# Optimization experiments

Measured on AMD Instinct MI355X. Metric: run time of the kernel, lower is better.

The kernel has to match this reference:

```python
import jax, jax.numpy as jnp
import numpy as np

NZ = 128
N_GEN = 8
BATCH = 2048
SLOPE = 0.2


def _convt(x, w, b, stride, pad):
    # PyTorch ConvTranspose2d(weight [Cin,Cout,kH,kW], stride, padding p)
    # == conv with lhs_dilation=stride, padding=k-1-p, spatially-flipped
    # kernel with in/out channels swapped.
    k = jnp.flip(w, axis=(2, 3)).transpose(2, 3, 0, 1)  # [kH,kW,Cin,Cout]
    y = jax.lax.conv_general_dilated(
        x, k, window_strides=(1, 1), padding=[(pad, pad), (pad, pad)],
        lhs_dilation=(stride, stride),
        dimension_numbers=('NCHW', 'HWIO', 'NCHW'))
    return y + b[None, :, None, None]


def setup_inputs() -> dict:
    key = jax.random.key(0)
    ks = jax.random.split(key, 12)
    s = 0.05
    return {
        'z': jax.random.normal(ks[0], (BATCH, NZ), jnp.float32),
        'g_idx': jax.random.randint(ks[1], (BATCH,), 0, N_GEN),
        'W1': jax.random.normal(ks[2], (N_GEN, NZ, 256), jnp.float32) * s,
        'b1': jax.random.normal(ks[3], (N_GEN, 256), jnp.float32) * s,
        'W2': jax.random.normal(ks[4], (N_GEN, 256, 1568), jnp.float32) * s,
        'b2': jax.random.normal(ks[5], (N_GEN, 1568), jnp.float32) * s,
        'cw1': jax.random.normal(ks[6], (N_GEN, 32, 16, 4, 4), jnp.float32) * s,
        'cb1': jax.random.normal(ks[7], (N_GEN, 16), jnp.float32) * s,
        'cw2': jax.random.normal(ks[8], (N_GEN, 16, 8, 4, 4), jnp.float32) * s,
        'cb2': jax.random.normal(ks[9], (N_GEN, 8), jnp.float32) * s,
        'cw3': jax.random.normal(ks[10], (N_GEN, 8, 1, 3, 3), jnp.float32) * s,
        'cb3': jax.random.normal(ks[11], (N_GEN, 1), jnp.float32) * s,
    }


def _single_gen(params, z):
    W1, b1, W2, b2, cw1, cb1, cw2, cb2, cw3, cb3 = params
    lrelu = lambda x: jax.nn.leaky_relu(x, SLOPE)
    h = lrelu(z @ W1 + b1)                 # [B,256]
    h = lrelu(h @ W2 + b2)                 # [B,1568]
    h = h.reshape(-1, 32, 7, 7)
    h = lrelu(_convt(h, cw1, cb1, 2, 2))   # [B,16,14,14]
    h = lrelu(_convt(h, cw2, cb2, 2, 2))   # [B,8,28,28]
    return jnp.tanh(_convt(h, cw3, cb3, 1, 1))  # [B,1,28,28]


def reference(z, g_idx, W1, b1, W2, b2, cw1, cb1, cw2, cb2, cw3, cb3):
    params = (W1, b1, W2, b2, cw1, cb1, cw2, cb2, cw3, cb3)
    # Compute every generator on the full batch (faithful to the torch loop),
    # vmapped over the generator axis: images [G,B,1,28,28].
    images = jax.vmap(_single_gen, in_axes=((0,) * 10, None))(params, z)
    # Per-sample gather: keep generator g_idx[b] for each sample b.
    return images[g_idx, jnp.arange(z.shape[0])]
```

## Files before the change

### kernel.cpp

```cpp
#include <hip/hip_runtime.h>
#include <cstdint>
#include <cstddef>

#define BATCH 2048
#define NZ 128
#define NGEN 8
#define GRPS 32
#define MAXG 72
#define NCT 7
#define H2_ELEMS 1792
#define WS_H1_OFF 16384
#define WS_H2_OFF (16384 + MAXG * 8192 * 4)
#define WS_W2T_OFF (WS_H2_OFF + BATCH * H2_ELEMS * 2)
#define W2T_GSTRIDE (1568 * 256)
#define NB_W2T (NGEN * 49)
#define NB_PREP (NB_W2T + MAXG * 4)
#define WS_WPK1_OFF (WS_W2T_OFF + NGEN * W2T_GSTRIDE * 2)
#define WS_WPK2_OFF (WS_WPK1_OFF + NGEN * 8192 * 2)
#define WS_WPK3_OFF (WS_WPK2_OFF + NGEN * 1024 * 4)
#define PS 304

typedef unsigned int u32;
typedef unsigned short u16;
typedef unsigned long long u64;
typedef _Float16 f16x8 __attribute__((ext_vector_type(8)));
typedef _Float16 f16x4 __attribute__((ext_vector_type(4)));
typedef _Float16 f16x2 __attribute__((ext_vector_type(2)));
typedef float f32x4 __attribute__((ext_vector_type(4)));

__device__ __forceinline__ float lrelu(float x) { return fmaxf(x, 0.2f * x); }
__device__ __forceinline__ u16 f16b(float f) {
    _Float16 h = (_Float16)f;
    return __builtin_bit_cast(u16, h);
}
__device__ __forceinline__ u32 pk2(float a, float b) {
    f16x2 v; v[0] = (_Float16)a; v[1] = (_Float16)b;
    return __builtin_bit_cast(u32, v);
}
__device__ __forceinline__ float dot2(u32 a, u32 b, float c) {
#if __has_builtin(__builtin_amdgcn_fdot2)
    return __builtin_amdgcn_fdot2(__builtin_bit_cast(f16x2, a),
                                  __builtin_bit_cast(f16x2, b), c, false);
#else
    float d;
    asm("v_dot2_f32_f16 %0, %1, %2, %3" : "=v"(d) : "v"(a), "v"(b), "v"(c));
    return d;
#endif
}
__device__ __forceinline__ float fast_tanh(float x) {
    x = fminf(fmaxf(x, -9.f), 9.f);
    const float e = __expf(2.f * x);
    return (e - 1.f) / (e + 1.f);
}
__device__ __forceinline__ int h2off(int n) {
    const int ci = n / 49, rm = n % 49;
    return ci * 56 + (rm / 7) * 8 + (rm % 7);
}

__global__ __launch_bounds__(256) void prep_kernel(
    const float* __restrict__ z, const int* __restrict__ g_idx,
    const float* __restrict__ W1, const float* __restrict__ b1,
    const float* __restrict__ W2, int* __restrict__ wsi,
    float* __restrict__ h1g, _Float16* __restrict__ W2T,
    const float* __restrict__ cw1, const float* __restrict__ cw2,
    const float* __restrict__ cw3,
    u16* __restrict__ apk1, u32* __restrict__ wpk2, u32* __restrict__ wpk3)
{
    __shared__ __align__(16) char pmem[16896];

    const int tid = threadIdx.x;
    const int bx = blockIdx.x;

    if (bx < NB_W2T) {
        _Float16 (*t)[264] = (_Float16 (*)[264])pmem;
        const int g = bx / 49;
        const int n0 = (bx % 49) * 32;
        const float* src = W2 + (size_t)g * 256 * 1568;
        const int nl = tid & 31, kh = tid >> 5;
        #pragma unroll 8
        for (int p = 0; p < 32; ++p) {
            const int k = p * 8 + kh;
            t[nl][k] = (_Float16)src[(size_t)k * 1568 + n0 + nl];
        }
        __syncthreads();
        _Float16* dst = W2T + (size_t)g * W2T_GSTRIDE + (size_t)n0 * 256;
        #pragma unroll
        for (int ii = 0; ii < 4; ++ii) {
            const int i = tid + 256 * ii;
            const int n = i >> 5, kc = i & 31;
            *(uint4*)(dst + (size_t)n * 256 + kc * 8) = *(const uint4*)&t[n][kc * 8];
        }
        return;
    }

    if (bx >= NB_PREP && bx < NB_PREP + NGEN) {
        const int g = bx - NB_PREP;
        const float* c1p = cw1 + g * 8192;
        u16* o1 = apk1 + g * 8192;
        for (int i = tid; i < 8192; i += 256) {
            const int ci = i & 31, co = (i >> 5) & 15, t = (i >> 9) & 3;
            const int px = (i >> 11) & 1, py = (i >> 12) & 1;
            const int a = 1 - py + 2 * (t >> 1);
            const int c = 1 - px + 2 * (t & 1);
            o1[i] = f16b(c1p[ci * 256 + co * 16 + a * 4 + c]);
        }
        const float* c2p = cw2 + g * 2048;
        u32* o2 = wpk2 + g * 1024;
        for (int i = tid; i < 1024; i += 256) {
            const int cip = i >> 7, a = (i >> 5) & 3, co = (i >> 2) & 7, c = i & 3;
            const float* s = c2p + cip * 256 + co * 16 + a * 4 + c;
            o2[i] = pk2(s[0], s[128]);
        }
        if (tid < 36) {
            const int cip = tid / 9, r = tid % 9;
            const float* s = cw3 + g * 72 + cip * 18 + r;
            wpk3[g * 36 + tid] = pk2(s[0], s[9]);
        }
        return;
    }

    u16* rank       = (u16*)pmem;
    int (*wcnt)[NGEN]  = (int (*)[NGEN])(pmem + 4096);
    int (*wboff)[NGEN] = (int (*)[NGEN])(pmem + 4224);
    int* pbase      = (int*)(pmem + 4352);
    const int w = tid >> 6, lane = tid & 63;
    if (tid < 4 * NGEN) wcnt[tid >> 3][tid & 7] = 0;
    __syncthreads();
    const u64 lt = ((u64)1 << lane) - 1;
    #pragma unroll
    for (int r = 0; r < 8; ++r) {
        const int b = r * 256 + tid;
        const int gg = g_idx[b];
        u64 m[NGEN];
        #pragma unroll
        for (int k = 0; k < NGEN; ++k) m[k] = __ballot(gg == k);
        rank[b] = (u16)((int)__popcll(m[gg] & lt) + wcnt[w][gg]);
        if (lane < NGEN) wcnt[w][lane] += (int)__popcll(m[lane]);
    }
    __syncthreads();
    if (tid == 0) {
        int acc = 0;
        for (int g = 0; g < NGEN; ++g) {
            pbase[g] = acc;
            const int tot = wcnt[0][g] + wcnt[1][g] + wcnt[2][g] + wcnt[3][g];
            acc += ((tot + GRPS - 1) / GRPS) * GRPS;
        }
        pbase[NGEN] = acc;
    }
    __syncthreads();
    if (tid < 32) {
        const int ww = tid >> 3, g = tid & 7;
        int off = pbase[g];
        for (int w2 = 0; w2 < ww; ++w2) off += wcnt[w2][g];
        wboff[ww][g] = off;
    }
    __syncthreads();

    if (bx >= NB_PREP + NGEN) {
        if (tid == 0) wsi[0] = pbase[NGEN];
        for (int i = tid; i < MAXG * GRPS; i += 256) wsi[16 + i] = -1;
        __syncthreads();
        #pragma unroll
        for (int r = 0; r < 8; ++r) {
            const int b = r * 256 + tid;
            const int gg = g_idx[b];
            wsi[16 + wboff[w][gg] + (int)rank[b]] = b;
        }
        return;
    }

    const int bx2 = bx - NB_W2T;
    const int grp = bx2 >> 2;
    const int s0 = (bx2 & 3) * 8;
    if (grp * GRPS >= pbase[NGEN]) return;

    int gsel = 0;
    #pragma unroll
    for (int g = 1; g < NGEN; ++g) if (grp * GRPS >= pbase[g]) gsel = g;

    int* sb = (int*)(pmem + 4400);
    float (*zst)[12] = (float (*)[12])(pmem + 4608);
    if (tid < 8) sb[tid] = -1;
    __syncthreads();
    const int base = grp * GRPS + s0;
    #pragma unroll
    for (int r = 0; r < 8; ++r) {
        const int b = r * 256 + tid;
        const int gg = g_idx[b];
        const int rel = wboff[w][gg] + (int)rank[b] - base;
        if ((unsigned)rel < 8u) sb[rel] = b;
    }
    __syncthreads();

    const float* W1g = W1 + gsel * (NZ * 256);
    const float* b1g = b1 + gsel * 256;

    {
        const int s = tid >> 5, f = tid & 31;
        float4 v = make_float4(0.f, 0.f, 0.f, 0.f);
        if (sb[s] >= 0) v = *(const float4*)(z + (size_t)sb[s] * NZ + 4 * f);
        zst[4 * f + 0][s] = v.x; zst[4 * f + 1][s] = v.y;
        zst[4 * f + 2][s] = v.z; zst[4 * f + 3][s] = v.w;
    }
    __syncthreads();

    const int c = tid;
    float acc[8];
    #pragma unroll
    for (int s = 0; s < 8; ++s) acc[s] = 0.f;
    const float* wp = W1g + c;
    #pragma unroll 4
    for (int k = 0; k < NZ; ++k) {
        const float wv = wp[k * 256];
        float av[8];
        *(float4*)&av[0] = *(const float4*)&zst[k][0];
        *(float4*)&av[4] = *(const float4*)&zst[k][4];
        #pragma unroll
        for (int s = 0; s < 8; ++s) acc[s] += av[s] * wv;
    }
    const float bv = b1g[c];
    float* hp = h1g + (size_t)grp * 8192 + (size_t)s0 * 256 + c;
    #pragma unroll
    for (int s = 0; s < 8; ++s) hp[s * 256] = lrelu(acc[s] + bv);
}

__global__ __launch_bounds__(256) void fc2_kernel(
    const int* __restrict__ g_idx,
    const _Float16* __restrict__ W2T, const float* __restrict__ b2,
    const int* __restrict__ wsi, const float* __restrict__ h1g,
    u16* __restrict__ h2g)
{
    __shared__ __align__(16) char afsm[GRPS * PS * 2];
    _Float16* afrag = (_Float16*)afsm;
    __shared__ int sb[GRPS];
    __shared__ int sG;

    const int tid = threadIdx.x;
    const int grp = blockIdx.x / NCT;
    const int tile = blockIdx.x % NCT;
    if (grp * GRPS >= wsi[0]) return;

    if (tid == 0) sG = g_idx[wsi[16 + grp * GRPS]];
    if (tid < GRPS) sb[tid] = wsi[16 + grp * GRPS + tid];
    __syncthreads();
    const _Float16* W2Tg = W2T + (size_t)sG * W2T_GSTRIDE;
    const float* b2g = b2 + sG * 1568;

    {
        const float4* h1p4 = (const float4*)(h1g + (size_t)grp * 8192);
        #pragma unroll
        for (int i = 0; i < 8; ++i) {
            const int u = tid + 256 * i;
            const int j4 = u & 1;
            const int ln = (u >> 1) & 63;
            const int kq = (u >> 7) & 7;
            const int mt = (u >> 10) & 1;
            const int s = mt * 16 + (ln & 15);
            const float4 v = h1p4[s * 64 + kq * 8 + ((ln >> 4) << 1) + j4];
            f16x4 hi;
            hi[0] = (_Float16)v.x; hi[1] = (_Float16)v.y;
            hi[2] = (_Float16)v.z; hi[3] = (_Float16)v.w;
            const int bh = ((mt * 8 + kq) * 64 + ln) * 8 + 4 * j4;
            *(f16x4*)&afrag[bh] = hi;
        }
    }
    __syncthreads();

    const int wave = tid >> 6;
    const int lane = tid & 63;
    const int q = lane >> 4;
    const int nl = lane & 15;
    const int nbw = tile * 256 + wave * 64;

    f32x4 accA[4], accB[4];
    #pragma unroll
    for (int nt = 0; nt < 4; ++nt) {
        accA[nt] = (f32x4){0.f, 0.f, 0.f, 0.f};
        accB[nt] = accA[nt];
    }
    #pragma unroll
    for (int nt = 0; nt < 4; ++nt) {
        const int nb = nbw + nt * 16;
        if (nb < 1568) {
            const _Float16* bp = W2Tg + (size_t)(nb + nl) * 256 + q * 8;
            #pragma unroll
            for (int kq = 0; kq < 8; ++kq) {
                const f16x8 b = *(const f16x8*)(bp + kq * 32);
                const f16x8 a0 = *(const f16x8*)&afrag[((0 * 8 + kq) * 64 + lane) * 8];
                const f16x8 a1 = *(const f16x8*)&afrag[((1 * 8 + kq) * 64 + lane) * 8];
                accA[nt] = __builtin_amdgcn_mfma_f32_16x16x32_f16(a0, b, accA[nt], 0, 0, 0);
                accB[nt] = __builtin_amdgcn_mfma_f32_16x16x32_f16(a1, b, accB[nt], 0, 0, 0);
            }
        }
    }
    __syncthreads();

    u16* pst = (u16*)afsm;
    const int nstart = tile * 256;
    const int nend = (nstart + 256 < 1568) ? nstart + 256 : 1568;
    const int offLo = h2off(nstart), offHi = h2off(nend - 1);
    const int lo8 = offLo & ~7;

    #pragma unroll
    for (int nt = 0; nt < 4; ++nt) {
        const int nb = nbw + nt * 16;
        if (nb < 1568) {
            const int n = nb + nl;
            const float bias = b2g[n];
            u16* pp = pst + (h2off(n) - lo8);
            #pragma unroll
            for (int reg = 0; reg < 4; ++reg) {
                pp[(q * 4 + reg) * PS]      = f16b(lrelu(accA[nt][reg] + bias));
                pp[(16 + q * 4 + reg) * PS] = f16b(lrelu(accB[nt][reg] + bias));
            }
        }
    }
    __syncthreads();

    {
        const int s = tid >> 3, p = tid & 7;
        const int bb = sb[s];
        if (bb >= 0) {
            u16* row = h2g + (size_t)bb * H2_ELEMS;
            const u16* ps = pst + s * PS - lo8;
            const int c0 = (offLo + 7) & ~7;
            const int c1 = (offHi + 1) & ~7;
            for (int o = offLo + p; o < c0 && o <= offHi; o += 8) row[o] = ps[o];
            const int t0 = (c1 > offLo) ? c1 : offLo;
            for (int o = t0 + p; o <= offHi; o += 8) row[o] = ps[o];
            for (int c = c0 + p * 8; c + 8 <= c1; c += 64)
                *(uint4*)(row + c) = *(const uint4*)(ps + c);
        }
    }
}

__device__ __forceinline__ void conv2p_full(
    const u32 (*c1s)[14][20], u16* dst,
    const u32* __restrict__ w2g, const float bv, const int co, const int y)
{
    float acc[28];
    #pragma unroll
    for (int x = 0; x < 28; ++x) acc[x] = bv;
    const int a0 = (y + 1) & 1;
    for (int aa = 0; aa < 2; ++aa) {
        const int a = a0 + 2 * aa;
        const int iy = (y + 1 - a) >> 1;
        if ((unsigned)iy < 14u) {
            #pragma unroll 2
            for (int cip = 0; cip < 8; ++cip) {
                u32 rr[14];
                *(uint4*)&rr[0]  = *(const uint4*)&c1s[cip][iy][0];
                *(uint4*)&rr[4]  = *(const uint4*)&c1s[cip][iy][4];
                *(uint4*)&rr[8]  = *(const uint4*)&c1s[cip][iy][8];
                *(uint2*)&rr[12] = *(const uint2*)&c1s[cip][iy][12];
                const uint4 wq = *(const uint4*)(w2g + ((cip * 4 + a) * 8 + co) * 4);
                const u32 wv[4] = {wq.x, wq.y, wq.z, wq.w};
                #pragma unroll
                for (int x = 0; x < 28; ++x) {
                    const int c0v = (x + 1) & 1;
                    const int ix0 = (x + 1 - c0v) >> 1;
                    if (ix0 < 14) acc[x] = dot2(rr[ix0],     wv[c0v],     acc[x]);
                    if (ix0 >= 1) acc[x] = dot2(rr[ix0 - 1], wv[c0v + 2], acc[x]);
                }
            }
        }
    }
    #pragma unroll
    for (int x = 0; x < 28; ++x) dst[2 * (1 + x)] = f16b(lrelu(acc[x]));
}

__global__ __launch_bounds__(256, 6) void conv_kernel(
    const int* __restrict__ g_idx, const int* __restrict__ wsi,
    const u16* __restrict__ apk1, const float* __restrict__ cb1,
    const u32* __restrict__ wpk2, const float* __restrict__ cb2,
    const u32* __restrict__ wpk3, const float* __restrict__ cb3,
    const u16* __restrict__ h2g, float* __restrict__ out)
{
    __shared__ __align__(16) char smem[8960 + 13440];
    u32 (*c1s)[14][20] = (u32 (*)[14][20])smem;
    u32 (*h2s)[9][10]  = (u32 (*)[9][10])(smem + 8960);
    u32 (*c2s)[28][30] = (u32 (*)[28][30])(smem + 8960);
    __shared__ u32 w3s[36];
    __shared__ float sc1[16];

    const int tid = threadIdx.x;
    const int b = wsi[16 + blockIdx.x];
    if (b < 0) return;
    const int g = g_idx[b];
    const u16* a1g = apk1 + g * 8192;
    const u32* w2g = wpk2 + g * 1024;
    const float* cb2g = cb2 + g * 8;
    const float  cb3v = cb3[g];

    for (int i = tid; i < 656; i += 256) {
        const int cip = i / 41, rem = i % 41;
        int r, c;
        if (rem < 10)      { r = 0; c = rem; }
        else if (rem < 20) { r = 8; c = rem - 10; }
        else { const int j = rem - 20; r = 1 + j / 3;
               const int jm = j % 3; c = (jm == 0) ? 0 : (jm == 1 ? 8 : 9); }
        h2s[cip][r][c] = 0u;
    }
    if (tid < 224) {
        const uint4 qv = ((const uint4*)(h2g + (size_t)b * H2_ELEMS))[tid];
        const int ci = tid / 7, yq = tid % 7;
        u16* dst = (u16*)&h2s[ci >> 1][yq + 1][1] + (ci & 1);
        const u32 w[4] = {qv.x, qv.y, qv.z, qv.w};
        #pragma unroll
        for (int j = 0; j < 3; ++j) {
            dst[4 * j]     = (u16)(w[j] & 0xffffu);
            dst[4 * j + 2] = (u16)(w[j] >> 16);
        }
        dst[12] = (u16)(w[3] & 0xffffu);
    }
    if (tid < 36) w3s[tid] = wpk3[g * 36 + tid];
    if (tid < 16) sc1[tid] = cb1[g * 16 + tid];
    __syncthreads();

    {
        const int wv_ = tid >> 6;
        const int py = wv_ >> 1, px = wv_ & 1;
        const int lane = tid & 63;
        const int n = lane & 15;
        const int q = lane >> 4;
        const u16* ag = a1g + ((py * 2 + px) * 4) * 512 + n * 32 + q * 8;
        f16x8 af[4];
        #pragma unroll
        for (int t = 0; t < 4; ++t) af[t] = *(const f16x8*)(ag + t * 512);

        int oyv[4], oxv[4];
        #pragma unroll
        for (int tile = 0; tile < 4; ++tile) {
            int p = tile * 16 + n; if (p > 48) p = 48;
            oyv[tile] = p / 7; oxv[tile] = p % 7;
        }
        f32x4 acc[4];
        #pragma unroll
        for (int tile = 0; tile < 4; ++tile) acc[tile] = (f32x4){0.f, 0.f, 0.f, 0.f};

        #pragma unroll
        for (int t = 0; t < 4; ++t) {
            const int dy = py - (t >> 1) + 1;
            const int dx = px - (t & 1) + 1;
            #pragma unroll
            for (int tile = 0; tile < 4; ++tile) {
                const int r = oyv[tile] + dy, c = oxv[tile] + dx;
                uint4 bw;
                bw.x = h2s[q * 4 + 0][r][c];
                bw.y = h2s[q * 4 + 1][r][c];
                bw.z = h2s[q * 4 + 2][r][c];
                bw.w = h2s[q * 4 + 3][r][c];
                acc[tile] = __builtin_amdgcn_mfma_f32_16x16x32_f16(
                    af[t], __builtin_bit_cast(f16x8, bw), acc[tile], 0, 0, 0);
            }
        }
        #pragma unroll
        for (int tile = 0; tile < 4; ++tile) {
            const int pos = tile * 16 + n;
            if (pos < 49) {
                const int y = 2 * oyv[tile] + py, x = 2 * oxv[tile] + px;
                #pragma unroll
                for (int reg = 0; reg < 4; ++reg) {
                    const int m = q * 4 + reg;
                    u16* d = (u16*)&c1s[m >> 1][y][x] + (m & 1);
                    *d = f16b(lrelu(acc[tile][reg] + sc1[m]));
                }
            }
        }
    }
    __syncthreads();

    if (tid < 224) {
        const int zc = tid / 56, zr = tid % 56;
        c2s[zc][zr % 28][(zr < 28) ? 0 : 29] = 0u;
        const int co = tid / 28, y = tid % 28;
        const float bv = cb2g[co];
        u16* dst = (u16*)&c2s[co >> 1][y][0] + (co & 1);
        conv2p_full(c1s, dst, w2g, bv, co, y);
    }
    __syncthreads();

    if (tid < 196) {
        const int y = tid / 7, qq = tid % 7;
        const int xb = qq * 4;
        float acc[4] = {cb3v, cb3v, cb3v, cb3v};
        #pragma unroll 2
        for (int cip = 0; cip < 4; ++cip) {
            u32 wp[9];
            #pragma unroll
            for (int j = 0; j < 9; ++j) wp[j] = w3s[cip * 9 + j];
            #pragma unroll
            for (int a = 0; a < 3; ++a) {
                const int iy = y + 1 - a;
                if ((unsigned)iy < 28u) {
                    u32 rr[6];
                    *(uint2*)&rr[0] = *(const uint2*)&c2s[cip][iy][xb];
                    *(uint2*)&rr[2] = *(const uint2*)&c2s[cip][iy][xb + 2];
                    *(uint2*)&rr[4] = *(const uint2*)&c2s[cip][iy][xb + 4];
                    #pragma unroll
                    for (int xx = 0; xx < 4; ++xx)
                        #pragma unroll
                        for (int c = 0; c < 3; ++c)
                            acc[xx] = dot2(rr[xx + 2 - c], wp[a * 3 + c], acc[xx]);
                }
            }
        }
        float* op = out + (size_t)b * 784 + y * 28 + xb;
        #pragma unroll
        for (int xx = 0; xx < 4; ++xx) op[xx] = fast_tanh(acc[xx]);
    }
}

extern "C" void kernel_launch(void* const* d_in, const int* in_sizes, int n_in,
                              void* d_out, int out_size, void* d_ws, size_t ws_size,
                              hipStream_t stream) {
    const float* z   = (const float*)d_in[0];
    const int*   gi  = (const int*)d_in[1];
    const float* W1  = (const float*)d_in[2];
    const float* b1  = (const float*)d_in[3];
    const float* W2  = (const float*)d_in[4];
    const float* b2  = (const float*)d_in[5];
    const float* cw1 = (const float*)d_in[6];
    const float* cb1 = (const float*)d_in[7];
    const float* cw2 = (const float*)d_in[8];
    const float* cb2 = (const float*)d_in[9];
    const float* cw3 = (const float*)d_in[10];
    const float* cb3 = (const float*)d_in[11];
    int*      wsi = (int*)d_ws;
    float*    h1g = (float*)((char*)d_ws + WS_H1_OFF);
    u16*      h2g = (u16*)((char*)d_ws + WS_H2_OFF);
    _Float16* w2t = (_Float16*)((char*)d_ws + WS_W2T_OFF);
    u16*      apk1 = (u16*)((char*)d_ws + WS_WPK1_OFF);
    u32*      wpk2 = (u32*)((char*)d_ws + WS_WPK2_OFF);
    u32*      wpk3 = (u32*)((char*)d_ws + WS_WPK3_OFF);

    prep_kernel<<<NB_PREP + NGEN + 1, 256, 0, stream>>>(z, gi, W1, b1, W2, wsi,
                                                        h1g, w2t, cw1, cw2, cw3,
                                                        apk1, wpk2, wpk3);
    fc2_kernel<<<MAXG * NCT, 256, 0, stream>>>(gi, w2t, b2, wsi, h1g, h2g);
    conv_kernel<<<MAXG * GRPS, 256, 0, stream>>>(gi, wsi, apk1, cb1, wpk2, cb2,
                                                 wpk3, cb3, h2g, (float*)d_out);
}
```

Baseline: 148.4 us.

## Compute second transposed conv with MFMA instead of per-thread dot2 loops

Replaces the scalar dot2-based second transposed convolution with a sub-pixel decomposition running on 16x16x32 f16 MFMA. Each of the four waves handles one output parity. The weights are repacked in prep into zero-padded A fragments with 16 output channels, of which 8 are real, and the conv1 output is stored in a padded [row][cip][col] layout so B fragments can be gathered. This removes a long serial accumulation that used only 224 threads. In exchange, half of the MFMA output rows are wasted on padding, and the B-operand gathers from shared memory are strided.

Result: no change. 147.4 us (-0.7%).

```diff
diff --git a/kernel.cpp b/kernel.cpp
--- a/kernel.cpp
+++ b/kernel.cpp
@@ -16,8 +16,8 @@
 #define NB_W2T (NGEN * 49)
 #define NB_PREP (NB_W2T + MAXG * 4)
 #define WS_WPK1_OFF (WS_W2T_OFF + NGEN * W2T_GSTRIDE * 2)
-#define WS_WPK2_OFF (WS_WPK1_OFF + NGEN * 8192 * 2)
-#define WS_WPK3_OFF (WS_WPK2_OFF + NGEN * 1024 * 4)
+#define WS_APK2_OFF (WS_WPK1_OFF + NGEN * 8192 * 2)
+#define WS_WPK3_OFF (WS_APK2_OFF + NGEN * 4096 * 2)
 #define PS 304
 
 typedef unsigned int u32;
@@ -64,7 +64,7 @@
     float* __restrict__ h1g, _Float16* __restrict__ W2T,
     const float* __restrict__ cw1, const float* __restrict__ cw2,
     const float* __restrict__ cw3,
-    u16* __restrict__ apk1, u32* __restrict__ wpk2, u32* __restrict__ wpk3)
+    u16* __restrict__ apk1, u16* __restrict__ apk2, u32* __restrict__ wpk3)
 {
     __shared__ __align__(16) char pmem[16896];
 
@@ -105,11 +105,15 @@
             o1[i] = f16b(c1p[ci * 256 + co * 16 + a * 4 + c]);
         }
         const float* c2p = cw2 + g * 2048;
-        u32* o2 = wpk2 + g * 1024;
-        for (int i = tid; i < 1024; i += 256) {
-            const int cip = i >> 7, a = (i >> 5) & 3, co = (i >> 2) & 7, c = i & 3;
-            const float* s = c2p + cip * 256 + co * 16 + a * 4 + c;
-            o2[i] = pk2(s[0], s[128]);
+        u16* o2 = apk2 + g * 4096;
+        for (int i = tid; i < 4096; i += 256) {
+            const int k = i & 31, co = (i >> 5) & 15;
+            const int pair = (i >> 9) & 1, par = (i >> 10) & 3;
+            const int py = par >> 1, px = par & 1;
+            const int t2 = k >> 4, ci = k & 15;
+            const int a = 1 - py + 2 * pair;
+            const int ccol = 1 - px + 2 * t2;
+            o2[i] = (co < 8) ? f16b(c2p[ci * 128 + co * 16 + a * 4 + ccol]) : (u16)0;
         }
         if (tid < 36) {
             const int cip = tid / 9, r = tid % 9;
@@ -334,62 +338,27 @@
     }
 }
 
-__device__ __forceinline__ void conv2p_full(
-    const u32 (*c1s)[14][20], u16* dst,
-    const u32* __restrict__ w2g, const float bv, const int co, const int y)
-{
-    float acc[28];
-    #pragma unroll
-    for (int x = 0; x < 28; ++x) acc[x] = bv;
-    const int a0 = (y + 1) & 1;
-    for (int aa = 0; aa < 2; ++aa) {
-        const int a = a0 + 2 * aa;
-        const int iy = (y + 1 - a) >> 1;
-        if ((unsigned)iy < 14u) {
-            #pragma unroll 2
-            for (int cip = 0; cip < 8; ++cip) {
-                u32 rr[14];
-                *(uint4*)&rr[0]  = *(const uint4*)&c1s[cip][iy][0];
-                *(uint4*)&rr[4]  = *(const uint4*)&c1s[cip][iy][4];
-                *(uint4*)&rr[8]  = *(const uint4*)&c1s[cip][iy][8];
-                *(uint2*)&rr[12] = *(const uint2*)&c1s[cip][iy][12];
-                const uint4 wq = *(const uint4*)(w2g + ((cip * 4 + a) * 8 + co) * 4);
-                const u32 wv[4] = {wq.x, wq.y, wq.z, wq.w};
-                #pragma unroll
-                for (int x = 0; x < 28; ++x) {
-                    const int c0v = (x + 1) & 1;
-                    const int ix0 = (x + 1 - c0v) >> 1;
-                    if (ix0 < 14) acc[x] = dot2(rr[ix0],     wv[c0v],     acc[x]);
-                    if (ix0 >= 1) acc[x] = dot2(rr[ix0 - 1], wv[c0v + 2], acc[x]);
-                }
-            }
-        }
-    }
-    #pragma unroll
-    for (int x = 0; x < 28; ++x) dst[2 * (1 + x)] = f16b(lrelu(acc[x]));
-}
-
 __global__ __launch_bounds__(256, 6) void conv_kernel(
     const int* __restrict__ g_idx, const int* __restrict__ wsi,
     const u16* __restrict__ apk1, const float* __restrict__ cb1,
-    const u32* __restrict__ wpk2, const float* __restrict__ cb2,
+    const u16* __restrict__ apk2, const float* __restrict__ cb2,
     const u32* __restrict__ wpk3, const float* __restrict__ cb3,
     const u16* __restrict__ h2g, float* __restrict__ out)
 {
-    __shared__ __align__(16) char smem[8960 + 13440];
-    u32 (*c1s)[14][20] = (u32 (*)[14][20])smem;
-    u32 (*h2s)[9][10]  = (u32 (*)[9][10])(smem + 8960);
-    u32 (*c2s)[28][30] = (u32 (*)[28][30])(smem + 8960);
+    __shared__ __align__(16) char smem[8704 + 13440];
+    u32 (*c1w)[8][17]  = (u32 (*)[8][17])smem;
+    u32 (*h2s)[9][10]  = (u32 (*)[9][10])(smem + 8704);
+    u32 (*c2s)[28][30] = (u32 (*)[28][30])(smem + 8704);
     __shared__ u32 w3s[36];
     __shared__ float sc1[16];
+    __shared__ float sc2[8];
 
     const int tid = threadIdx.x;
     const int b = wsi[16 + blockIdx.x];
     if (b < 0) return;
     const int g = g_idx[b];
     const u16* a1g = apk1 + g * 8192;
-    const u32* w2g = wpk2 + g * 1024;
-    const float* cb2g = cb2 + g * 8;
+    const u16* a2g = apk2 + g * 4096;
     const float  cb3v = cb3[g];
 
     for (int i = tid; i < 656; i += 256) {
@@ -401,6 +370,14 @@
                const int jm = j % 3; c = (jm == 0) ? 0 : (jm == 1 ? 8 : 9); }
         h2s[cip][r][c] = 0u;
     }
+    for (int i = tid; i < 496; i += 256) {
+        int r, cip, c;
+        if (i < 272) { r = (i < 136) ? 0 : 15; const int rem = i % 136;
+                       cip = rem / 17; c = rem % 17; }
+        else { const int j = i - 272; r = 1 + (j >> 4); const int k2 = j & 15;
+               cip = k2 >> 1; c = (k2 & 1) ? 15 : 0; }
+        c1w[r][cip][c] = 0u;
+    }
     if (tid < 224) {
         const uint4 qv = ((const uint4*)(h2g + (size_t)b * H2_ELEMS))[tid];
         const int ci = tid / 7, yq = tid % 7;
@@ -415,14 +392,16 @@
     }
     if (tid < 36) w3s[tid] = wpk3[g * 36 + tid];
     if (tid < 16) sc1[tid] = cb1[g * 16 + tid];
-    __syncthreads();
+    if (tid < 8)  sc2[tid] = cb2[g * 8 + tid];
+    __syncthreads();
+
+    const int wv_ = tid >> 6;
+    const int py = wv_ >> 1, px = wv_ & 1;
+    const int lane = tid & 63;
+    const int n = lane & 15;
+    const int q = lane >> 4;
 
     {
-        const int wv_ = tid >> 6;
-        const int py = wv_ >> 1, px = wv_ & 1;
-        const int lane = tid & 63;
-        const int n = lane & 15;
-        const int q = lane >> 4;
         const u16* ag = a1g + ((py * 2 + px) * 4) * 512 + n * 32 + q * 8;
         f16x8 af[4];
         #pragma unroll
@@ -462,7 +441,7 @@
                 #pragma unroll
                 for (int reg = 0; reg < 4; ++reg) {
                     const int m = q * 4 + reg;
-                    u16* d = (u16*)&c1s[m >> 1][y][x] + (m & 1);
+                    u16* d = (u16*)&c1w[y + 1][m >> 1][x + 1] + (m & 1);
                     *d = f16b(lrelu(acc[tile][reg] + sc1[m]));
                 }
             }
@@ -470,13 +449,54 @@
     }
     __syncthreads();
 
-    if (tid < 224) {
-        const int zc = tid / 56, zr = tid % 56;
-        c2s[zc][zr % 28][(zr < 28) ? 0 : 29] = 0u;
-        const int co = tid / 28, y = tid % 28;
-        const float bv = cb2g[co];
-        u16* dst = (u16*)&c2s[co >> 1][y][0] + (co & 1);
-        conv2p_full(c1s, dst, w2g, bv, co, y);
+    {
+        if (tid < 224) {
+            const int zc = tid / 56, zr = tid % 56;
+            c2s[zc][zr % 28][(zr < 28) ? 0 : 29] = 0u;
+        }
+        const u16* ag2 = a2g + (py * 2 + px) * 1024 + n * 32 + q * 8;
+        const f16x8 af0 = *(const f16x8*)(ag2);
+        const f16x8 af1 = *(const f16x8*)(ag2 + 512);
+        const int t2 = q >> 1;
+        const int cipb = (q & 1) * 4;
+
+        #pragma unroll
+        for (int tile = 0; tile < 13; ++tile) {
+            const int pos = tile * 16 + n;
+            const int pv = (pos < 196) ? pos : 195;
+            const int oy = pv / 14, ox = pv % 14;
+            const int c = ox + px - t2 + 1;
+            f32x4 acc = {0.f, 0.f, 0.f, 0.f};
+            {
+                const int r = oy + py + 1;
+                uint4 bw;
+                bw.x = c1w[r][cipb + 0][c];
+                bw.y = c1w[r][cipb + 1][c];
+                bw.z = c1w[r][cipb + 2][c];
+                bw.w = c1w[r][cipb + 3][c];
+                acc = __builtin_amdgcn_mfma_f32_16x16x32_f16(
+                    af0, __builtin_bit_cast(f16x8, bw), acc, 0, 0, 0);
+            }
+            {
+                const int r = oy + py;
+                uint4 bw;
+                bw.x = c1w[r][cipb + 0][c];
+                bw.y = c1w[r][cipb + 1][c];
+                bw.z = c1w[r][cipb + 2][c];
+                bw.w = c1w[r][cipb + 3][c];
+                acc = __builtin_amdgcn_mfma_f32_16x16x32_f16(
+                    af1, __builtin_bit_cast(f16x8, bw), acc, 0, 0, 0);
+            }
+            if (pos < 196 && q < 2) {
+                const int y = 2 * oy + py, x = 2 * ox + px;
+                #pragma unroll
+                for (int reg = 0; reg < 4; ++reg) {
+                    const int co = q * 4 + reg;
+                    u16* d = (u16*)&c2s[co >> 1][y][1 + x] + (co & 1);
+                    *d = f16b(lrelu(acc[reg] + sc2[co]));
+                }
+            }
+        }
     }
     __syncthreads();
 
@@ -531,13 +551,13 @@
     u16*      h2g = (u16*)((char*)d_ws + WS_H2_OFF);
     _Float16* w2t = (_Float16*)((char*)d_ws + WS_W2T_OFF);
     u16*      apk1 = (u16*)((char*)d_ws + WS_WPK1_OFF);
-    u32*      wpk2 = (u32*)((char*)d_ws + WS_WPK2_OFF);
+    u16*      apk2 = (u16*)((char*)d_ws + WS_APK2_OFF);
     u32*      wpk3 = (u32*)((char*)d_ws + WS_WPK3_OFF);
 
     prep_kernel<<<NB_PREP + NGEN + 1, 256, 0, stream>>>(z, gi, W1, b1, W2, wsi,
                                                         h1g, w2t, cw1, cw2, cw3,
-                                                        apk1, wpk2, wpk3);
+                                                        apk1, apk2, wpk3);
     fc2_kernel<<<MAXG * NCT, 256, 0, stream>>>(gi, w2t, b2, wsi, h1g, h2g);
-    conv_kernel<<<MAXG * GRPS, 256, 0, stream>>>(gi, wsi, apk1, cb1, wpk2, cb2,
+    conv_kernel<<<MAXG * GRPS, 256, 0, stream>>>(gi, wsi, apk1, cb1, apk2, cb2,
                                                  wpk3, cb3, h2g, (float*)d_out);
 }
```
